# Kernel tuning notes

Measured on AMD Instinct MI355X. Metric: run time of the kernel, lower is better.

## Reference

```python
import jax, jax.numpy as jnp
import numpy as np

B, N, PAST = 2, 1024, 1024
DIM, HEADS, DH = 2048, 16, 128
INNER = HEADS * DH
LN_EPS = 1e-5
ROPE_THETA = 10000.0


def setup_inputs() -> dict:
    key = jax.random.key(0)
    k0, k1, k2, k3, k4 = jax.random.split(key, 5)
    x = jax.random.normal(k0, (B, N, DIM), dtype=jnp.float32)
    past_k = jax.random.normal(k1, (B, HEADS, PAST, DH), dtype=jnp.float32)
    past_v = jax.random.normal(k2, (B, HEADS, PAST, DH), dtype=jnp.float32)
    # causal mask with KV-cache offset: query i sits at global pos PAST+i,
    # mask (True = blocked) keys at positions j > PAST+i
    kv = PAST + N
    q_pos = PAST + jnp.arange(N)
    k_pos = jnp.arange(kv)
    mask = jnp.broadcast_to((k_pos[None, :] > q_pos[:, None])[None, None], (B, 1, N, kv))
    w_qkv = jax.random.normal(k3, (DIM, 3 * INNER), dtype=jnp.float32) * (DIM ** -0.5)
    w_out = jax.random.normal(k4, (INNER, DIM), dtype=jnp.float32) * (INNER ** -0.5)
    ln_g = jnp.ones((DIM,), dtype=jnp.float32)
    ln_b = jnp.zeros((DIM,), dtype=jnp.float32)
    return {"x": x, "past_k": past_k, "past_v": past_v, "mask": mask,
            "w_qkv": w_qkv, "w_out": w_out, "ln_g": ln_g, "ln_b": ln_b}


def _layernorm(x, g, b):
    mu = jnp.mean(x, axis=-1, keepdims=True)
    var = jnp.mean((x - mu) ** 2, axis=-1, keepdims=True)
    return (x - mu) * jax.lax.rsqrt(var + LN_EPS) * g + b


def _rope(t, pos):
    # interleaved rotary (lucidrains rotary-embedding-torch convention)
    inv_freq = 1.0 / (ROPE_THETA ** (jnp.arange(0, DH, 2, dtype=jnp.float32) / DH))
    freqs = pos.astype(jnp.float32)[:, None] * inv_freq[None, :]   # [n, DH/2]
    freqs = jnp.repeat(freqs, 2, axis=-1)                          # [n, DH]
    cos = jnp.cos(freqs).astype(t.dtype)
    sin = jnp.sin(freqs).astype(t.dtype)
    t2 = t.reshape(*t.shape[:-1], DH // 2, 2)
    rot = jnp.stack((-t2[..., 1], t2[..., 0]), axis=-1).reshape(t.shape)
    return t * cos + rot * sin


def reference(x, past_k, past_v, mask, w_qkv, w_out, ln_g, ln_b):
    b, n, _ = x.shape
    xn = _layernorm(x, ln_g, ln_b)
    qkv = xn @ w_qkv                                               # [b, n, 3*INNER]
    q, k, v = jnp.split(qkv, 3, axis=-1)
    to_heads = lambda t: t.reshape(b, n, HEADS, DH).transpose(0, 2, 1, 3)  # b h n d
    q, k, v = to_heads(q), to_heads(k), to_heads(v)
    k = jnp.concatenate((past_k, k), axis=2)                       # [b, h, kv, d]
    v = jnp.concatenate((past_v, v), axis=2)
    kv_len = k.shape[2]
    q = _rope(q, jnp.arange(n) + (kv_len - n))
    k = _rope(k, jnp.arange(kv_len))
    scale = DH ** -0.5
    dots = jnp.einsum('bhnd,bhmd->bhnm', q, k) * scale             # [b, h, n, kv]
    dots = jnp.where(mask, -jnp.inf, dots)
    attn = jax.nn.softmax(dots, axis=-1)
    out = jnp.einsum('bhnm,bhmd->bhnd', attn, v)                   # [b, h, n, d]
    out = out.transpose(0, 2, 1, 3).reshape(b, n, INNER)
    return out @ w_out, k, v
```

## Files before the change

kernel.cpp:

```cpp
#include <hip/hip_runtime.h>
#include <hip/hip_bf16.h>
#include <math.h>

#define BB    2
#define NN    1024
#define PAST  1024
#define KVL   2048
#define DIM   2048
#define HEADS 16
#define DH    128
#define INNER 2048
#define NQKV  6144
#define TOK   2048
#define LN_EPS 1e-5f

typedef __attribute__((ext_vector_type(8))) short   short8;
typedef __attribute__((ext_vector_type(4))) float   f32x4;
typedef __attribute__((ext_vector_type(8))) unsigned short us8;
typedef __attribute__((ext_vector_type(4))) unsigned short us4;
typedef unsigned short us;

__device__ __forceinline__ float bfbits2f(us u) {
    return __uint_as_float(((unsigned int)u) << 16);
}
__device__ __forceinline__ us f2bfb(float f) {
    union { __hip_bfloat16 h; us u; } cv;
    cv.h = __float2bfloat16(f);
    return cv.u;
}
__device__ __forceinline__ us8 pack8u(float4 a, float4 b) {
    us8 r;
    r[0] = f2bfb(a.x); r[1] = f2bfb(a.y); r[2] = f2bfb(a.z); r[3] = f2bfb(a.w);
    r[4] = f2bfb(b.x); r[5] = f2bfb(b.y); r[6] = f2bfb(b.z); r[7] = f2bfb(b.w);
    return r;
}

__device__ __forceinline__ void gload_lds16(const void* gsrc, void* ldst) {
    __builtin_amdgcn_global_load_lds(
        (const __attribute__((address_space(1))) void*)gsrc,
        (__attribute__((address_space(3))) void*)ldst, 16, 0, 0);
}

__global__ __launch_bounds__(256) void transp_kernel(
    const float* __restrict__ src, us* __restrict__ dst, int R, int C)
{
    const int c0 = blockIdx.x * 64;
    const int r0 = blockIdx.y * 64;
    const int tid = threadIdx.x;

    __shared__ us T[64][68];

    #pragma unroll
    for (int e = 0; e < 4; e++) {
        int idx = tid + e * 256;
        int jr  = idx >> 4;
        int c4  = (idx & 15) * 4;
        float4 v = *reinterpret_cast<const float4*>(
            src + (size_t)(r0 + jr) * C + c0 + c4);
        us4 w;
        w[0] = f2bfb(v.x); w[1] = f2bfb(v.y); w[2] = f2bfb(v.z); w[3] = f2bfb(v.w);
        *reinterpret_cast<us4*>(&T[jr][c4]) = w;
    }
    __syncthreads();

    #pragma unroll
    for (int e = 0; e < 4; e++) {
        int idx = tid + e * 256;
        int d   = idx >> 4;
        int k4  = (idx & 15) * 4;
        us4 w;
        w[0] = T[k4 + 0][d];
        w[1] = T[k4 + 1][d];
        w[2] = T[k4 + 2][d];
        w[3] = T[k4 + 3][d];
        *reinterpret_cast<us4*>(dst + (size_t)(c0 + d) * R + r0 + k4) = w;
    }
}

__global__ __launch_bounds__(256) void ln_kernel(
    const float* __restrict__ x, const float* __restrict__ g,
    const float* __restrict__ b, us* __restrict__ xn)
{
    const int t   = blockIdx.x;
    const int tid = threadIdx.x;
    const size_t base = (size_t)t * DIM;

    float4 p0 = reinterpret_cast<const float4*>(x + base)[tid * 2 + 0];
    float4 p1 = reinterpret_cast<const float4*>(x + base)[tid * 2 + 1];
    float v[8] = {p0.x, p0.y, p0.z, p0.w, p1.x, p1.y, p1.z, p1.w};

    float s1 = 0.f, s2 = 0.f;
    #pragma unroll
    for (int i = 0; i < 8; i++) { s1 += v[i]; s2 += v[i] * v[i]; }

    #pragma unroll
    for (int off = 32; off; off >>= 1) {
        s1 += __shfl_xor(s1, off);
        s2 += __shfl_xor(s2, off);
    }
    __shared__ float red1[4], red2[4];
    if ((tid & 63) == 0) { red1[tid >> 6] = s1; red2[tid >> 6] = s2; }
    __syncthreads();
    float S1 = red1[0] + red1[1] + red1[2] + red1[3];
    float S2 = red2[0] + red2[1] + red2[2] + red2[3];
    const float inv = 1.0f / (float)DIM;
    float mu  = S1 * inv;
    float var = S2 * inv - mu * mu;
    float rstd = rsqrtf(var + LN_EPS);

    const int d0 = tid * 8;
    float4 oa, ob;
    oa.x = (v[0] - mu) * rstd * g[d0 + 0] + b[d0 + 0];
    oa.y = (v[1] - mu) * rstd * g[d0 + 1] + b[d0 + 1];
    oa.z = (v[2] - mu) * rstd * g[d0 + 2] + b[d0 + 2];
    oa.w = (v[3] - mu) * rstd * g[d0 + 3] + b[d0 + 3];
    ob.x = (v[4] - mu) * rstd * g[d0 + 4] + b[d0 + 4];
    ob.y = (v[5] - mu) * rstd * g[d0 + 5] + b[d0 + 5];
    ob.z = (v[6] - mu) * rstd * g[d0 + 6] + b[d0 + 6];
    ob.w = (v[7] - mu) * rstd * g[d0 + 7] + b[d0 + 7];

    *reinterpret_cast<us8*>(xn + base + d0) = pack8u(oa, ob);
}

template<bool OUT_BF16>
__global__ __launch_bounds__(256) void gemm_bt_kernel(
    const us* __restrict__ A, const us* __restrict__ Bt,
    void* __restrict__ Cout, int M, int N, int K)
{
    __shared__ us As[128][40];
    __shared__ us Bs[128][40];

    const int tid  = threadIdx.x;
    const int wave = tid >> 6, lane = tid & 63;
    const int quad = lane >> 4, l16 = lane & 15;
    const int wm = wave & 1, wn = wave >> 1;
    const int m0 = blockIdx.y * 128, n0 = blockIdx.x * 128;

    f32x4 acc[4][4];
    #pragma unroll
    for (int i = 0; i < 4; i++)
        #pragma unroll
        for (int j = 0; j < 4; j++)
            #pragma unroll
            for (int r = 0; r < 4; r++) acc[i][j][r] = 0.f;

    const int s_row = tid >> 2;
    const int s_c8  = (tid & 3) * 8;

    const us* pa0 = A  + (size_t)(m0 + s_row)      * K + s_c8;
    const us* pa1 = A  + (size_t)(m0 + 64 + s_row) * K + s_c8;
    const us* pb0 = Bt + (size_t)(n0 + s_row)      * K + s_c8;
    const us* pb1 = Bt + (size_t)(n0 + 64 + s_row) * K + s_c8;

    for (int k0 = 0; k0 < K; k0 += 32) {
        us8 a0 = *reinterpret_cast<const us8*>(pa0 + k0);
        us8 a1 = *reinterpret_cast<const us8*>(pa1 + k0);
        us8 b0 = *reinterpret_cast<const us8*>(pb0 + k0);
        us8 b1 = *reinterpret_cast<const us8*>(pb1 + k0);

        __syncthreads();
        *reinterpret_cast<us8*>(&As[s_row][s_c8])      = a0;
        *reinterpret_cast<us8*>(&As[64 + s_row][s_c8]) = a1;
        *reinterpret_cast<us8*>(&Bs[s_row][s_c8])      = b0;
        *reinterpret_cast<us8*>(&Bs[64 + s_row][s_c8]) = b1;
        __syncthreads();

        short8 af[4], bf[4];
        #pragma unroll
        for (int mi = 0; mi < 4; mi++)
            af[mi] = *reinterpret_cast<const short8*>(
                &As[wm * 64 + mi * 16 + l16][quad * 8]);
        #pragma unroll
        for (int ni = 0; ni < 4; ni++)
            bf[ni] = *reinterpret_cast<const short8*>(
                &Bs[wn * 64 + ni * 16 + l16][quad * 8]);

        #pragma unroll
        for (int mi = 0; mi < 4; mi++)
            #pragma unroll
            for (int ni = 0; ni < 4; ni++)
                acc[mi][ni] = __builtin_amdgcn_mfma_f32_16x16x32_bf16(
                    af[mi], bf[ni], acc[mi][ni], 0, 0, 0);
    }

    #pragma unroll
    for (int mi = 0; mi < 4; mi++) {
        #pragma unroll
        for (int r = 0; r < 4; r++) {
            size_t row = (size_t)(m0 + wm * 64 + mi * 16 + quad * 4 + r);
            #pragma unroll
            for (int ni = 0; ni < 4; ni++) {
                size_t col = n0 + wn * 64 + ni * 16 + l16;
                if (OUT_BF16)
                    ((us*)Cout)[row * N + col] = f2bfb(acc[mi][ni][r]);
                else
                    ((float*)Cout)[row * N + col] = acc[mi][ni][r];
            }
        }
    }
}

__global__ __launch_bounds__(256) void rope_kernel(
    const float* __restrict__ past_k, const float* __restrict__ past_v,
    us* __restrict__ qkv, float* __restrict__ out_k, float* __restrict__ out_v,
    us* __restrict__ Kbf)
{
    const int tid  = threadIdx.x;
    const int pid  = blockIdx.x * 4 + (tid >> 6);
    const int lane = tid & 63;

    const int b   = pid / (HEADS * KVL);
    const int rem = pid - b * (HEADS * KVL);
    const int h   = rem / KVL;
    const int pos = rem - h * KVL;

    const float invf = exp2f((float)lane * (-13.287712379549449f / 64.0f));
    float sn, cs;
    sincosf((float)pos * invf, &sn, &cs);

    const size_t obase = ((size_t)(b * HEADS + h) * KVL + pos) * DH + 2 * lane;

    float k0, k1;
    if (pos < PAST) {
        const size_t pbase = ((size_t)(b * HEADS + h) * PAST + pos) * DH + 2 * lane;
        k0 = past_k[pbase];
        k1 = past_k[pbase + 1];
    } else {
        const int t = b * NN + (pos - PAST);
        const us* qp = qkv + (size_t)t * NQKV + INNER + h * DH + 2 * lane;
        k0 = bfbits2f(qp[0]); k1 = bfbits2f(qp[1]);
    }
    float kr0 = k0 * cs - k1 * sn;
    float kr1 = k1 * cs + k0 * sn;
    out_k[obase]     = kr0;
    out_k[obase + 1] = kr1;
    Kbf[obase]       = f2bfb(kr0);
    Kbf[obase + 1]   = f2bfb(kr1);

    if (pos < PAST) {
        const size_t pbase = ((size_t)(b * HEADS + h) * PAST + pos) * DH + 2 * lane;
        out_v[obase]     = past_v[pbase];
        out_v[obase + 1] = past_v[pbase + 1];
    } else {
        const int t = b * NN + (pos - PAST);
        const us* vp = qkv + (size_t)t * NQKV + 2 * INNER + h * DH + 2 * lane;
        out_v[obase]     = bfbits2f(vp[0]);
        out_v[obase + 1] = bfbits2f(vp[1]);
    }

    if (pos >= PAST) {
        const int t = b * NN + (pos - PAST);
        us* qq = qkv + (size_t)t * NQKV + h * DH + 2 * lane;
        float q0 = bfbits2f(qq[0]), q1 = bfbits2f(qq[1]);
        qq[0] = f2bfb(q0 * cs - q1 * sn);
        qq[1] = f2bfb(q1 * cs + q0 * sn);
    }
}

__global__ __launch_bounds__(256) void vtrans_kernel(
    const float* __restrict__ Vc, us* __restrict__ Vtg)
{
    const int jb = blockIdx.x;
    const int db = blockIdx.y;
    const int bh = blockIdx.z;
    const int tid = threadIdx.x;

    __shared__ us T[64][68];

    const float* src = Vc + ((size_t)bh * KVL + jb * 64) * DH + db * 64;
    #pragma unroll
    for (int e = 0; e < 4; e++) {
        int idx = tid + e * 256;
        int jr  = idx >> 4;
        int c4  = (idx & 15) * 4;
        float4 v = *reinterpret_cast<const float4*>(src + (size_t)jr * DH + c4);
        us4 w;
        w[0] = f2bfb(v.x); w[1] = f2bfb(v.y); w[2] = f2bfb(v.z); w[3] = f2bfb(v.w);
        *reinterpret_cast<us4*>(&T[jr][c4]) = w;
    }
    __syncthreads();

    us* dst = Vtg + ((size_t)bh * DH + db * 64) * KVL + jb * 64;
    #pragma unroll
    for (int e = 0; e < 4; e++) {
        int idx = tid + e * 256;
        int d   = idx >> 4;
        int k4  = (idx & 15) * 4;
        us4 w;
        w[0] = T[k4 + 0][d];
        w[1] = T[k4 + 1][d];
        w[2] = T[k4 + 2][d];
        w[3] = T[k4 + 3][d];
        *reinterpret_cast<us4*>(dst + (size_t)d * KVL + k4) = w;
    }
}

__global__ __launch_bounds__(256) void attn_mfma_kernel(
    const us* __restrict__ qkv,
    const us* __restrict__ Kbf,
    const us* __restrict__ Vtg,
    us* __restrict__ Ao)
{
    const int qt   = blockIdx.x;
    const int h    = blockIdx.y;
    const int b    = blockIdx.z;
    const int tid  = threadIdx.x;
    const int wave = tid >> 6;
    const int lane = tid & 63;
    const int quad = lane >> 4;
    const int l16  = lane & 15;

    __shared__ us Ks[2][64 * 128];
    __shared__ us Vt[2][128 * 64];
    __shared__ us Pb[64][72];

    short8 qf[4];
    {
        const int qrow = qt * 64 + wave * 16 + l16;
        const us* qp = qkv + (size_t)(b * NN + qrow) * NQKV + h * DH;
        #pragma unroll
        for (int ks = 0; ks < 4; ks++)
            qf[ks] = *reinterpret_cast<const short8*>(qp + ks * 32 + quad * 8);
    }

    f32x4 Oacc[8];
    #pragma unroll
    for (int t = 0; t < 8; t++)
        #pragma unroll
        for (int r = 0; r < 4; r++) Oacc[t][r] = 0.f;
    float mrow[4] = {-INFINITY, -INFINITY, -INFINITY, -INFINITY};
    float lrow[4] = {0.f, 0.f, 0.f, 0.f};

    const us* kptr = Kbf + (size_t)(b * HEADS + h) * KVL * DH;
    const us* vtb  = Vtg + (size_t)(b * HEADS + h) * DH * KVL;
    const float scale = 0.08838834764831845f;
    const int qg = PAST + qt * 64 + wave * 16 + quad * 4;
    const int nch = 17 + qt;

    auto stage = [&](int j0, int buf) {
        #pragma unroll
        for (int e = 0; e < 4; e++) {
            int phys = (e * 256 + tid) * 16;
            int row  = phys >> 8;
            int col  = (phys & 255) ^ ((row & 7) << 4);
            gload_lds16((const char*)(kptr + (size_t)(j0 + row) * DH) + col,
                        (char*)&Ks[buf][0] + phys);
        }
        #pragma unroll
        for (int e = 0; e < 4; e++) {
            int phys = (e * 256 + tid) * 16;
            int row  = phys >> 7;
            int col  = (phys & 127) ^ ((row & 7) << 4);
            gload_lds16((const char*)(vtb + (size_t)row * KVL + j0) + col,
                        (char*)&Vt[buf][0] + phys);
        }
    };

    stage(0, 0);
    __syncthreads();

    int cur = 0;
    for (int c = 0; c < nch; c++) {
        const int j0 = c * 64;
        if (c + 1 < nch) stage(j0 + 64, cur ^ 1);

        f32x4 S[4];
        #pragma unroll
        for (int t = 0; t < 4; t++)
            #pragma unroll
            for (int r = 0; r < 4; r++) S[t][r] = 0.f;
        __builtin_amdgcn_s_setprio(1);
        #pragma unroll
        for (int ks = 0; ks < 4; ks++) {
            #pragma unroll
            for (int t = 0; t < 4; t++) {
                int row  = t * 16 + l16;
                int colb = ks * 64 + quad * 16;
                const char* p = (const char*)&Ks[cur][0] +
                                row * 256 + (colb ^ ((row & 7) << 4));
                short8 kb = *reinterpret_cast<const short8*>(p);
                S[t] = __builtin_amdgcn_mfma_f32_16x16x32_bf16(qf[ks], kb, S[t], 0, 0, 0);
            }
        }
        __builtin_amdgcn_s_setprio(0);

        #pragma unroll
        for (int t = 0; t < 4; t++) {
            int kg = j0 + t * 16 + l16;
            #pragma unroll
            for (int r = 0; r < 4; r++) {
                float s = S[t][r] * scale;
                S[t][r] = (kg <= qg + r) ? s : -INFINITY;
            }
        }

        float alpha[4];
        #pragma unroll
        for (int r = 0; r < 4; r++) {
            float mx = fmaxf(fmaxf(S[0][r], S[1][r]), fmaxf(S[2][r], S[3][r]));
            mx = fmaxf(mx, __shfl_xor(mx, 1));
            mx = fmaxf(mx, __shfl_xor(mx, 2));
            mx = fmaxf(mx, __shfl_xor(mx, 4));
            mx = fmaxf(mx, __shfl_xor(mx, 8));
            float nm = fmaxf(mrow[r], mx);
            alpha[r] = __expf(mrow[r] - nm);
            mrow[r] = nm;
            float rs = 0.f;
            #pragma unroll
            for (int t = 0; t < 4; t++) {
                float p = __expf(S[t][r] - nm);
                S[t][r] = p;
                rs += p;
            }
            rs += __shfl_xor(rs, 1);
            rs += __shfl_xor(rs, 2);
            rs += __shfl_xor(rs, 4);
            rs += __shfl_xor(rs, 8);
            lrow[r] = lrow[r] * alpha[r] + rs;
        }

        #pragma unroll
        for (int t = 0; t < 8; t++)
            #pragma unroll
            for (int r = 0; r < 4; r++) Oacc[t][r] *= alpha[r];

        #pragma unroll
        for (int t = 0; t < 4; t++)
            #pragma unroll
            for (int r = 0; r < 4; r++)
                Pb[wave * 16 + quad * 4 + r][t * 16 + l16] = f2bfb(S[t][r]);

        asm volatile("s_waitcnt lgkmcnt(0)" ::: "memory");
        __builtin_amdgcn_s_barrier();
        __builtin_amdgcn_sched_barrier(0);

        __builtin_amdgcn_s_setprio(1);
        #pragma unroll
        for (int kh = 0; kh < 2; kh++) {
            short8 pa = *reinterpret_cast<const short8*>(
                &Pb[wave * 16 + l16][kh * 32 + quad * 8]);
            #pragma unroll
            for (int t2 = 0; t2 < 8; t2++) {
                int row  = t2 * 16 + l16;
                int colb = kh * 64 + quad * 16;
                const char* p = (const char*)&Vt[cur][0] +
                                row * 128 + (colb ^ ((row & 7) << 4));
                short8 vb = *reinterpret_cast<const short8*>(p);
                Oacc[t2] = __builtin_amdgcn_mfma_f32_16x16x32_bf16(pa, vb, Oacc[t2], 0, 0, 0);
            }
        }
        __builtin_amdgcn_s_setprio(0);

        __syncthreads();
        cur ^= 1;
    }

    float invl[4];
    #pragma unroll
    for (int r = 0; r < 4; r++) invl[r] = 1.f / lrow[r];
    const int row0 = b * NN + qt * 64 + wave * 16 + quad * 4;
    #pragma unroll
    for (int r = 0; r < 4; r++) {
        us* dst = Ao + (size_t)(row0 + r) * INNER + h * DH + l16;
        #pragma unroll
        for (int t2 = 0; t2 < 8; t2++)
            dst[t2 * 16] = f2bfb(Oacc[t2][r] * invl[r]);
    }
}

extern "C" void kernel_launch(void* const* d_in, const int* in_sizes, int n_in,
                              void* d_out, int out_size, void* d_ws, size_t ws_size,
                              hipStream_t stream)
{
    const float* x      = (const float*)d_in[0];
    const float* past_k = (const float*)d_in[1];
    const float* past_v = (const float*)d_in[2];
    const float* w_qkv  = (const float*)d_in[4];
    const float* w_out  = (const float*)d_in[5];
    const float* ln_g   = (const float*)d_in[6];
    const float* ln_b   = (const float*)d_in[7];

    float* out   = (float*)d_out;
    float* out_k = out   + (size_t)BB * NN * DIM;
    float* out_v = out_k + (size_t)BB * HEADS * KVL * DH;

    us* xn   = (us*)d_ws;
    us* qkv  = xn  + (size_t)TOK * DIM;
    us* Wqt  = qkv + (size_t)TOK * NQKV;
    us* Wot  = Wqt + (size_t)NQKV * DIM;
    us* Vtg  = Wot + (size_t)DIM * INNER;
    us* attn = xn;
    us* Kbf  = Wqt;

    transp_kernel<<<dim3(NQKV / 64, DIM / 64), 256, 0, stream>>>(
        w_qkv, Wqt, DIM, NQKV);
    transp_kernel<<<dim3(DIM / 64, INNER / 64), 256, 0, stream>>>(
        w_out, Wot, INNER, DIM);

    ln_kernel<<<TOK, 256, 0, stream>>>(x, ln_g, ln_b, xn);

    gemm_bt_kernel<true><<<dim3(NQKV / 128, TOK / 128), 256, 0, stream>>>(
        xn, Wqt, (void*)qkv, TOK, NQKV, DIM);

    rope_kernel<<<(BB * HEADS * KVL) / 4, 256, 0, stream>>>(
        past_k, past_v, qkv, out_k, out_v, Kbf);

    vtrans_kernel<<<dim3(KVL / 64, DH / 64, BB * HEADS), 256, 0, stream>>>(
        out_v, Vtg);

    attn_mfma_kernel<<<dim3(NN / 64, HEADS, BB), 256, 0, stream>>>(
        qkv, Kbf, Vtg, attn);

    gemm_bt_kernel<false><<<dim3(DIM / 128, TOK / 128), 256, 0, stream>>>(
        attn, Wot, (void*)out, TOK, DIM, INNER);
}
```

Measured before the change: 421.4 us.

## Double-buffer GEMM via direct LDS loads; transpose S and lazily rescale softmax in attention

The GEMM now stages A/B tiles with async global-to-LDS loads into double buffers and prefetches the next K slice while running MFMAs, with raised wave priority around the MFMA block. In attention, the QK MFMA operands are swapped so each lane holds a full query row's scores. This removes most cross-lane shuffles for max and sum and lets P be written as packed vectors. Softmax rescaling is skipped unless the max grows by more than a threshold, and the row sum is reduced once at the end. The mid-loop barrier before the PV step is dropped, relying on each wave reading only its own rows of Pb. The lazy-rescale threshold risks fp32 overflow if scores jump by more than it.

```diff
diff --git a/kernel.cpp b/kernel.cpp
--- a/kernel.cpp
+++ b/kernel.cpp
@@ -127,8 +127,8 @@
     const us* __restrict__ A, const us* __restrict__ Bt,
     void* __restrict__ Cout, int M, int N, int K)
 {
-    __shared__ us As[128][40];
-    __shared__ us Bs[128][40];
+    __shared__ us As[2][128 * 32];
+    __shared__ us Bs[2][128 * 32];
 
     const int tid  = threadIdx.x;
     const int wave = tid >> 6, lane = tid & 63;
@@ -147,40 +147,44 @@
     const int s_row = tid >> 2;
     const int s_c8  = (tid & 3) * 8;
 
-    const us* pa0 = A  + (size_t)(m0 + s_row)      * K + s_c8;
-    const us* pa1 = A  + (size_t)(m0 + 64 + s_row) * K + s_c8;
-    const us* pb0 = Bt + (size_t)(n0 + s_row)      * K + s_c8;
-    const us* pb1 = Bt + (size_t)(n0 + 64 + s_row) * K + s_c8;
-
+    auto stage = [&](int k0, int buf) {
+        #pragma unroll
+        for (int e = 0; e < 2; e++) {
+            gload_lds16(A  + (size_t)(m0 + e * 64 + s_row) * K + k0 + s_c8,
+                        (char*)&As[buf][0] + (e * 256 + tid) * 16);
+            gload_lds16(Bt + (size_t)(n0 + e * 64 + s_row) * K + k0 + s_c8,
+                        (char*)&Bs[buf][0] + (e * 256 + tid) * 16);
+        }
+    };
+
+    stage(0, 0);
+    __syncthreads();
+
+    int buf = 0;
     for (int k0 = 0; k0 < K; k0 += 32) {
-        us8 a0 = *reinterpret_cast<const us8*>(pa0 + k0);
-        us8 a1 = *reinterpret_cast<const us8*>(pa1 + k0);
-        us8 b0 = *reinterpret_cast<const us8*>(pb0 + k0);
-        us8 b1 = *reinterpret_cast<const us8*>(pb1 + k0);
-
-        __syncthreads();
-        *reinterpret_cast<us8*>(&As[s_row][s_c8])      = a0;
-        *reinterpret_cast<us8*>(&As[64 + s_row][s_c8]) = a1;
-        *reinterpret_cast<us8*>(&Bs[s_row][s_c8])      = b0;
-        *reinterpret_cast<us8*>(&Bs[64 + s_row][s_c8]) = b1;
-        __syncthreads();
+        if (k0 + 32 < K) stage(k0 + 32, buf ^ 1);
 
         short8 af[4], bf[4];
         #pragma unroll
         for (int mi = 0; mi < 4; mi++)
             af[mi] = *reinterpret_cast<const short8*>(
-                &As[wm * 64 + mi * 16 + l16][quad * 8]);
+                &As[buf][(wm * 64 + mi * 16 + l16) * 32 + quad * 8]);
         #pragma unroll
         for (int ni = 0; ni < 4; ni++)
             bf[ni] = *reinterpret_cast<const short8*>(
-                &Bs[wn * 64 + ni * 16 + l16][quad * 8]);
-
+                &Bs[buf][(wn * 64 + ni * 16 + l16) * 32 + quad * 8]);
+
+        __builtin_amdgcn_s_setprio(1);
         #pragma unroll
         for (int mi = 0; mi < 4; mi++)
             #pragma unroll
             for (int ni = 0; ni < 4; ni++)
                 acc[mi][ni] = __builtin_amdgcn_mfma_f32_16x16x32_bf16(
                     af[mi], bf[ni], acc[mi][ni], 0, 0, 0);
+        __builtin_amdgcn_s_setprio(0);
+
+        __syncthreads();
+        buf ^= 1;
     }
 
     #pragma unroll
@@ -313,6 +317,7 @@
     __shared__ us Ks[2][64 * 128];
     __shared__ us Vt[2][128 * 64];
     __shared__ us Pb[64][72];
+    __shared__ float alF[4][16];
 
     short8 qf[4];
     {
@@ -328,13 +333,14 @@
     for (int t = 0; t < 8; t++)
         #pragma unroll
         for (int r = 0; r < 4; r++) Oacc[t][r] = 0.f;
-    float mrow[4] = {-INFINITY, -INFINITY, -INFINITY, -INFINITY};
-    float lrow[4] = {0.f, 0.f, 0.f, 0.f};
+    float m_run  = -INFINITY;
+    float l_part = 0.f;
 
     const us* kptr = Kbf + (size_t)(b * HEADS + h) * KVL * DH;
     const us* vtb  = Vtg + (size_t)(b * HEADS + h) * DH * KVL;
     const float scale = 0.08838834764831845f;
-    const int qg = PAST + qt * 64 + wave * 16 + quad * 4;
+    const float THRU  = 90.50966799f;
+    const int qg  = PAST + qt * 64 + wave * 16 + l16;
     const int nch = 17 + qt;
 
     auto stage = [&](int j0, int buf) {
@@ -379,59 +385,59 @@
                 const char* p = (const char*)&Ks[cur][0] +
                                 row * 256 + (colb ^ ((row & 7) << 4));
                 short8 kb = *reinterpret_cast<const short8*>(p);
-                S[t] = __builtin_amdgcn_mfma_f32_16x16x32_bf16(qf[ks], kb, S[t], 0, 0, 0);
+                S[t] = __builtin_amdgcn_mfma_f32_16x16x32_bf16(kb, qf[ks], S[t], 0, 0, 0);
             }
         }
         __builtin_amdgcn_s_setprio(0);
 
+        const int rel = qg - j0;
+        float mx = -INFINITY;
         #pragma unroll
         for (int t = 0; t < 4; t++) {
-            int kg = j0 + t * 16 + l16;
             #pragma unroll
             for (int r = 0; r < 4; r++) {
-                float s = S[t][r] * scale;
-                S[t][r] = (kg <= qg + r) ? s : -INFINITY;
+                int koff = t * 16 + quad * 4 + r;
+                S[t][r] = (koff <= rel) ? S[t][r] : -INFINITY;
+                mx = fmaxf(mx, S[t][r]);
             }
         }
-
-        float alpha[4];
-        #pragma unroll
-        for (int r = 0; r < 4; r++) {
-            float mx = fmaxf(fmaxf(S[0][r], S[1][r]), fmaxf(S[2][r], S[3][r]));
-            mx = fmaxf(mx, __shfl_xor(mx, 1));
-            mx = fmaxf(mx, __shfl_xor(mx, 2));
-            mx = fmaxf(mx, __shfl_xor(mx, 4));
-            mx = fmaxf(mx, __shfl_xor(mx, 8));
-            float nm = fmaxf(mrow[r], mx);
-            alpha[r] = __expf(mrow[r] - nm);
-            mrow[r] = nm;
-            float rs = 0.f;
-            #pragma unroll
-            for (int t = 0; t < 4; t++) {
-                float p = __expf(S[t][r] - nm);
-                S[t][r] = p;
+        mx = fmaxf(mx, __shfl_xor(mx, 16));
+        mx = fmaxf(mx, __shfl_xor(mx, 32));
+
+        float alpha = 1.f;
+        if (__any(mx > m_run + THRU)) {
+            float nm = fmaxf(m_run, mx);
+            alpha = __expf((m_run - nm) * scale);
+            m_run = nm;
+            if (quad == 0) alF[wave][l16] = alpha;
+            asm volatile("s_waitcnt lgkmcnt(0)" ::: "memory");
+            float a0 = alF[wave][quad * 4 + 0];
+            float a1 = alF[wave][quad * 4 + 1];
+            float a2 = alF[wave][quad * 4 + 2];
+            float a3 = alF[wave][quad * 4 + 3];
+            #pragma unroll
+            for (int t2 = 0; t2 < 8; t2++) {
+                Oacc[t2][0] *= a0; Oacc[t2][1] *= a1;
+                Oacc[t2][2] *= a2; Oacc[t2][3] *= a3;
+            }
+        }
+
+        const float nmk = -m_run * scale;
+        float rs = 0.f;
+        #pragma unroll
+        for (int t = 0; t < 4; t++) {
+            us4 w;
+            #pragma unroll
+            for (int r = 0; r < 4; r++) {
+                float p = __expf(fmaf(S[t][r], scale, nmk));
                 rs += p;
+                w[r] = f2bfb(p);
             }
-            rs += __shfl_xor(rs, 1);
-            rs += __shfl_xor(rs, 2);
-            rs += __shfl_xor(rs, 4);
-            rs += __shfl_xor(rs, 8);
-            lrow[r] = lrow[r] * alpha[r] + rs;
-        }
-
-        #pragma unroll
-        for (int t = 0; t < 8; t++)
-            #pragma unroll
-            for (int r = 0; r < 4; r++) Oacc[t][r] *= alpha[r];
-
-        #pragma unroll
-        for (int t = 0; t < 4; t++)
-            #pragma unroll
-            for (int r = 0; r < 4; r++)
-                Pb[wave * 16 + quad * 4 + r][t * 16 + l16] = f2bfb(S[t][r]);
+            *reinterpret_cast<us4*>(&Pb[wave * 16 + l16][t * 16 + quad * 4]) = w;
+        }
+        l_part = l_part * alpha + rs;
 
         asm volatile("s_waitcnt lgkmcnt(0)" ::: "memory");
-        __builtin_amdgcn_s_barrier();
         __builtin_amdgcn_sched_barrier(0);
 
         __builtin_amdgcn_s_setprio(1);
@@ -455,9 +461,13 @@
         cur ^= 1;
     }
 
+    l_part += __shfl_xor(l_part, 16);
+    l_part += __shfl_xor(l_part, 32);
     float invl[4];
     #pragma unroll
-    for (int r = 0; r < 4; r++) invl[r] = 1.f / lrow[r];
+    for (int r = 0; r < 4; r++)
+        invl[r] = 1.f / __shfl(l_part, quad * 4 + r);
+
     const int row0 = b * NN + qt * 64 + wave * 16 + quad * 4;
     #pragma unroll
     for (int r = 0; r < 4; r++) {
```

Result: faster. 381.3 us (-9.5%).
